# Optimization experiments

Hardware: AMD Instinct MI355X
Metric: run time of the kernel (lower is better)

## Reference

```python
import jax, jax.numpy as jnp
import numpy as np

NEG_INF = -1000000.0
B_, NG, HEADS, C, GH, GW, GD = 256, 64, 6, 192, 6, 6, 6
N = GH * GW * GD
POS_DIM = (C // 4) // 4  # DynamicPosBias(dim//4): pos_dim = (dim//4)//4 = 12


def setup_inputs() -> dict:
    key = jax.random.key(0)
    ks = jax.random.split(key, 12)
    rn = lambda k, shape, s=0.02: jax.random.normal(k, shape, jnp.float32) * s
    x = jax.random.normal(ks[0], (B_, N, C), jnp.float32)
    y = jax.random.normal(ks[1], (B_, N, C), jnp.float32)
    # 0 / -1e6 window mask, as produced by the padding logic upstream
    mask = jnp.where(jax.random.bernoulli(ks[2], 0.1, (NG, N, N)), NEG_INF, 0.0).astype(jnp.float32)
    return dict(
        x=x, y=y, mask=mask,
        Wqkv=rn(ks[3], (3 * C, C)), bqkv=jnp.zeros((3 * C,), jnp.float32),
        Wproj=rn(ks[4], (C, C)), bproj=jnp.zeros((C,), jnp.float32),
        pos_proj_w=rn(ks[5], (POS_DIM, 3)), pos_proj_b=jnp.zeros((POS_DIM,), jnp.float32),
        ln1_g=jnp.ones((POS_DIM,), jnp.float32), ln1_b=jnp.zeros((POS_DIM,), jnp.float32),
        pos1_w=rn(ks[6], (POS_DIM, POS_DIM)), pos1_b=jnp.zeros((POS_DIM,), jnp.float32),
        ln2_g=jnp.ones((POS_DIM,), jnp.float32), ln2_b=jnp.zeros((POS_DIM,), jnp.float32),
        pos2_w=rn(ks[7], (POS_DIM, POS_DIM)), pos2_b=jnp.zeros((POS_DIM,), jnp.float32),
        ln3_g=jnp.ones((POS_DIM,), jnp.float32), ln3_b=jnp.zeros((POS_DIM,), jnp.float32),
        pos3_w=rn(ks[8], (HEADS, POS_DIM)), pos3_b=jnp.zeros((HEADS,), jnp.float32),
        H=GH, W=GW, D=GD)


def _ln(t, g, b):
    m = t.mean(-1, keepdims=True)
    v = ((t - m) ** 2).mean(-1, keepdims=True)
    return (t - m) / jnp.sqrt(v + 1e-5) * g + b


def _rel_tables(H, W, D):
    # biases: all relative offsets in [1-H,H-1]x[1-W,W-1]x[1-D,D-1], shape (M, 3)
    ph = np.arange(1 - H, H); pw = np.arange(1 - W, W); pd = np.arange(1 - D, D)
    biases = np.stack(np.meshgrid(ph, pw, pd, indexing='ij')).reshape(3, -1).T.astype(np.float32)
    coords = np.stack(np.meshgrid(np.arange(H), np.arange(W), np.arange(D), indexing='ij')).reshape(3, -1)
    rel = (coords[:, :, None] - coords[:, None, :]).transpose(1, 2, 0)  # (N, N, 3)
    rel[..., 0] += H - 1; rel[..., 1] += W - 1; rel[..., 2] += D - 1
    rel[..., 0] *= (2 * W - 1) * (2 * D - 1); rel[..., 1] *= (2 * D - 1)
    idx = rel.sum(-1)  # (N, N) indices into the (M,) bias table
    return jnp.asarray(biases), jnp.asarray(idx)


def reference(x, y, mask, Wqkv, bqkv, Wproj, bproj, pos_proj_w, pos_proj_b,
              ln1_g, ln1_b, pos1_w, pos1_b, ln2_g, ln2_b, pos2_w, pos2_b,
              ln3_g, ln3_b, pos3_w, pos3_b, H, W, D):
    Bt, n, c = x.shape
    heads = pos3_w.shape[0]
    hd = c // heads
    scale = hd ** (-0.5)
    # NOTE: original code applies self.qkv to BOTH x and y (qkv_y layer unused)
    qkv = (x @ Wqkv.T + bqkv).reshape(Bt, n, 3, heads, hd).transpose(2, 0, 3, 1, 4)
    qkv_y = (y @ Wqkv.T + bqkv).reshape(Bt, n, 3, heads, hd).transpose(2, 0, 3, 1, 4)
    q = qkv[0] * scale
    k_y, v_y = qkv_y[1], qkv_y[2]
    attn = jnp.einsum('bhnd,bhmd->bhnm', q, k_y)
    # dynamic relative position bias: tiny MLP over offsets, then gather
    biases, idx = _rel_tables(H, W, D)
    pos = biases @ pos_proj_w.T + pos_proj_b
    pos = jnp.maximum(_ln(pos, ln1_g, ln1_b), 0) @ pos1_w.T + pos1_b
    pos = jnp.maximum(_ln(pos, ln2_g, ln2_b), 0) @ pos2_w.T + pos2_b
    pos = jnp.maximum(_ln(pos, ln3_g, ln3_b), 0) @ pos3_w.T + pos3_b  # (M, heads)
    rpb = pos[idx.reshape(-1)].reshape(n, n, heads).transpose(2, 0, 1)  # (heads, N, N)
    attn = attn + rpb[None]
    nG = mask.shape[0]
    attn = attn.reshape(Bt // nG, nG, heads, n, n) + mask[None, :, None]
    attn = jax.nn.softmax(attn, axis=-1).reshape(Bt, heads, n, n)
    out = jnp.einsum('bhnm,bhmd->bhnd', attn, v_y).transpose(0, 2, 1, 3).reshape(Bt, n, c)
    return out @ Wproj.T + bproj
```

## Files before the change

kernel.cpp:

```cpp
#include <hip/hip_runtime.h>
#include <stdint.h>

using short8   = __attribute__((ext_vector_type(8))) short;
using short4_  = __attribute__((ext_vector_type(4))) short;
using float4_  = __attribute__((ext_vector_type(4))) float;
using ushort4_ = __attribute__((ext_vector_type(4))) unsigned short;
typedef unsigned int  uint;
typedef unsigned short ushort;

__device__ __forceinline__ float bf2f(ushort b) {
  uint u = ((uint)b) << 16;
  return __builtin_bit_cast(float, u);
}
__device__ __forceinline__ ushort f2bf(float f) {
  uint u = __builtin_bit_cast(uint, f);
  u = u + 0x7fffu + ((u >> 16) & 1u);
  return (ushort)(u >> 16);
}
__device__ __forceinline__ float exp2_hw(float x) {
  float r;
  asm("v_exp_f32 %0, %1" : "=v"(r) : "v"(x));
  return r;
}
__device__ __forceinline__ void gld_lds16(const ushort* g, ushort* l) {
  __builtin_amdgcn_global_load_lds(
      (const __attribute__((address_space(1))) void*)g,
      (__attribute__((address_space(3))) void*)l, 16, 0, 0);
}
__device__ __forceinline__ int detect_f32(const uint* __restrict__ det) {
  int lane = threadIdx.x & 63;
  uint w = det[lane];
  ushort lo = (ushort)(w & 0xffffu);
  int e = (lo >> 7) & 0xff;
  int sane = (lo == 0 || (e >= 0x60 && e <= 0x9f)) ? 1 : 0;
  unsigned long long b = __ballot(sane);
  return (__popcll(b) >= 56) ? 0 : 1;
}

#define LOG2E 1.4426950408889634f

#define NN   216
#define NSQ  46656
#define PADV (-3.0e6f)

#if __has_builtin(__builtin_amdgcn_mfma_f32_16x16x16bf16_1k)
  #define HAVE_MFMA16 1
  #define MFMA16(a, b, c) __builtin_amdgcn_mfma_f32_16x16x16bf16_1k(a, b, c, 0, 0, 0)
#elif __has_builtin(__builtin_amdgcn_mfma_f32_16x16x16_bf16)
  #define HAVE_MFMA16 1
  #define MFMA16(a, b, c) __builtin_amdgcn_mfma_f32_16x16x16_bf16(a, b, c, 0, 0, 0)
#else
  #define HAVE_MFMA16 0
#endif

#define WA_WQKV   0
#define WA_BQKV   110592
#define WA_WPROJ  111168
#define WA_BPROJ  148032
#define WA_PPW    148224
#define WA_PPB    148260
#define WA_G1     148272
#define WA_B1     148284
#define WA_W1     148296
#define WA_WB1    148440
#define WA_G2     148452
#define WA_B2     148464
#define WA_W2     148476
#define WA_WB2    148620
#define WA_G3     148632
#define WA_B3     148644
#define WA_W3     148656
#define WA_WB3    148728
#define WA_TOTAL  148740

struct SrcPtrs { const void* p[18]; };

__global__ __launch_bounds__(256) void convpack_kernel(
    SrcPtrs sp, const uint* __restrict__ det,
    ushort* __restrict__ warena, ushort* __restrict__ wp) {
  int fl = detect_f32(det);
  int bid = blockIdx.x, tid = threadIdx.x;
  if (bid < 72) {
    int c = bid * 256 + tid;
    int blob = c / 2304, s = c - blob * 2304;
    int kk = s / 384, r = s - kk * 384;
    int nt = r >> 6, l = r & 63;
    int l16 = l & 15, qd = l >> 4;
    int col; const void* src;
    if (blob < 6) { int z = blob >> 1, half = blob & 1;
                    col = z * 192 + half * 96 + nt * 16 + l16; src = sp.p[0]; }
    else          { col = (blob - 6) * 96 + nt * 16 + l16;     src = sp.p[2]; }
    size_t off = (size_t)col * 192 + kk * 32 + qd * 8;
    short8 pk;
    if (fl) {
      float4_ lo = *(const float4_*)((const float*)src + off);
      float4_ hi = *(const float4_*)((const float*)src + off + 4);
#pragma unroll
      for (int j = 0; j < 4; ++j) {
        pk[j]     = (short)f2bf(lo[j]);
        pk[4 + j] = (short)f2bf(hi[j]);
      }
    } else {
      pk = *(const short8*)((const ushort*)src + off);
    }
    *(short8*)(wp + (size_t)c * 8) = pk;
  } else {
    constexpr int OFF[19] = {WA_WQKV, WA_BQKV, WA_WPROJ, WA_BPROJ, WA_PPW, WA_PPB,
                             WA_G1, WA_B1, WA_W1, WA_WB1, WA_G2, WA_B2, WA_W2,
                             WA_WB2, WA_G3, WA_B3, WA_W3, WA_WB3, WA_TOTAL};
    int u = (bid - 72) * 256 + tid;
    if (u >= 1284) return;
    int t, a;
    if (u < 576) { t = WA_BQKV + u; a = 1; }
    else {
      t = WA_BPROJ + (u - 576);
      a = 3;
#pragma unroll
      for (int i = 4; i < 18; ++i) a += (t >= OFF[i]) ? 1 : 0;
    }
    int local = t - OFF[a];
    const void* s = sp.p[a];
    warena[t] = fl ? f2bf(((const float*)s)[local]) : ((const ushort*)s)[local];
  }
}

__global__ __launch_bounds__(256) void packa_kernel(const void* __restrict__ src,
                                                    ushort* __restrict__ dst) {
  int fl = detect_f32((const uint*)src);
  int c = blockIdx.x * 256 + threadIdx.x;
  int tile = c / 3072, cc = c - tile * 3072;
  int kk = cc / 512, c2 = cc - kk * 512;
  int rowhi = c2 / 64, c3 = c2 - rowhi * 64;
  int q = c3 >> 4, l16 = c3 & 15;
  size_t M = (size_t)tile * 128 + rowhi * 16 + l16;
  size_t so = M * 192 + kk * 32 + q * 8;
  short8 pk;
  if (fl) {
    float4_ lo = *(const float4_*)((const float*)src + so);
    float4_ hi = *(const float4_*)((const float*)src + so + 4);
#pragma unroll
    for (int j = 0; j < 4; ++j) {
      pk[j]     = (short)f2bf(lo[j]);
      pk[4 + j] = (short)f2bf(hi[j]);
    }
  } else {
    pk = *(const short8*)((const ushort*)src + so);
  }
  *(short8*)(dst + (size_t)c * 8) = pk;
}

__device__ __forceinline__ void ln_relu(const float* p, const ushort* g,
                                        const ushort* b, float* r) {
  float m = 0.f;
#pragma unroll
  for (int t = 0; t < 12; ++t) m += p[t];
  m *= (1.f / 12.f);
  float v = 0.f;
#pragma unroll
  for (int t = 0; t < 12; ++t) { float d = p[t] - m; v += d * d; }
  v *= (1.f / 12.f);
  float inv = rsqrtf(v + 1e-5f);
#pragma unroll
  for (int t = 0; t < 12; ++t) {
    float z = (p[t] - m) * inv * bf2f(g[t]) + bf2f(b[t]);
    r[t] = fmaxf(z, 0.f);
  }
}

__global__ void pos_mlp_kernel(const ushort* __restrict__ wa, float* __restrict__ pos) {
  int m = blockIdx.x * blockDim.x + threadIdx.x;
  if (m >= 1331) return;
  const ushort* pw  = wa + WA_PPW;  const ushort* pb  = wa + WA_PPB;
  const ushort* g1  = wa + WA_G1;   const ushort* b1  = wa + WA_B1;
  const ushort* w1  = wa + WA_W1;   const ushort* wb1 = wa + WA_WB1;
  const ushort* g2  = wa + WA_G2;   const ushort* b2  = wa + WA_B2;
  const ushort* w2  = wa + WA_W2;   const ushort* wb2 = wa + WA_WB2;
  const ushort* g3  = wa + WA_G3;   const ushort* b3  = wa + WA_B3;
  const ushort* w3  = wa + WA_W3;   const ushort* wb3 = wa + WA_WB3;

  int ih = m / 121, rem = m - ih * 121;
  int iw = rem / 11, id = rem - iw * 11;
  float fh = (float)(ih - 5), fw = (float)(iw - 5), fd = (float)(id - 5);
  float p[12], r[12], q[12];
#pragma unroll
  for (int t = 0; t < 12; ++t)
    p[t] = fh * bf2f(pw[t * 3]) + fw * bf2f(pw[t * 3 + 1]) +
           fd * bf2f(pw[t * 3 + 2]) + bf2f(pb[t]);
  ln_relu(p, g1, b1, r);
#pragma unroll
  for (int t = 0; t < 12; ++t) {
    float s = bf2f(wb1[t]);
#pragma unroll
    for (int u = 0; u < 12; ++u) s += r[u] * bf2f(w1[t * 12 + u]);
    q[t] = s;
  }
  ln_relu(q, g2, b2, r);
#pragma unroll
  for (int t = 0; t < 12; ++t) {
    float s = bf2f(wb2[t]);
#pragma unroll
    for (int u = 0; u < 12; ++u) s += r[u] * bf2f(w2[t * 12 + u]);
    p[t] = s;
  }
  ln_relu(p, g3, b3, r);
#pragma unroll
  for (int h = 0; h < 6; ++h) {
    float s = bf2f(wb3[h]);
#pragma unroll
    for (int u = 0; u < 12; ++u) s += r[u] * bf2f(w3[h * 12 + u]);
    pos[m * 6 + h] = s;
  }
}

__global__ void rpbfrag_kernel(const float* __restrict__ pos, ushort* __restrict__ out) {
  int tgl = blockIdx.x * 256 + threadIdx.x;
  if (tgl >= 6 * 196 * 64) return;
  int lane = tgl & 63;
  int tj   = (tgl >> 6) % 196;
  int h    = (tgl >> 6) / 196;
  int tt = tj / 14, jt = tj - tt * 14;
  int l16 = lane & 15, quad = lane >> 4;
  int i = tt * 16 + l16;
  int jbase = jt * 16 + quad * 4;
  ushort4_ o;
  if (i < 216 && jbase < 216) {
    int h1 = i / 36, r1 = i - h1 * 36, w1 = r1 / 6, d1 = r1 - w1 * 6;
#pragma unroll
    for (int r = 0; r < 4; ++r) {
      int j = jbase + r;
      int h2 = j / 36, r2 = j - h2 * 36, w2 = r2 / 6, d2 = r2 - w2 * 6;
      int idx = ((h1 - h2 + 5) * 11 + (w1 - w2 + 5)) * 11 + (d1 - d2 + 5);
      o[r] = f2bf(pos[idx * 6 + h] * LOG2E);
    }
  } else {
#pragma unroll
    for (int r = 0; r < 4; ++r) o[r] = f2bf(PADV);
  }
  *(ushort4_*)(out + (size_t)tgl * 4) = o;
}

__global__ void maskfrag_kernel(const void* __restrict__ maskv,
                                const uint* __restrict__ det,
                                ushort* __restrict__ out) {
  bool mf32 = detect_f32(det) != 0;
  int tgl = blockIdx.x * 256 + threadIdx.x;
  if (tgl >= 64 * 196 * 64) return;
  int lane = tgl & 63;
  int tj   = (tgl >> 6) % 196;
  int g    = (tgl >> 6) / 196;
  int tt = tj / 14, jt = tj - tt * 14;
  int l16 = lane & 15, quad = lane >> 4;
  int i = tt * 16 + l16;
  int jbase = jt * 16 + quad * 4;
  ushort4_ o;
  if (i < 216 && jbase < 216) {
    int mi = i * 216 + jbase;
    if (mf32) {
      float4_ mv = *(const float4_*)((const float*)maskv + (size_t)g * NSQ + mi);
#pragma unroll
      for (int r = 0; r < 4; ++r) o[r] = f2bf(mv[r] * LOG2E);
    } else {
      ushort4_ raw = *(const ushort4_*)((const ushort*)maskv + (size_t)g * NSQ + mi);
#pragma unroll
      for (int r = 0; r < 4; ++r) o[r] = f2bf(bf2f(raw[r]) * LOG2E);
    }
  } else {
#pragma unroll
    for (int r = 0; r < 4; ++r) o[r] = f2bf(PADV);
  }
  *(ushort4_*)(out + (size_t)tgl * 4) = o;
}

template<int NT, int IS_PROJ>
__global__ __launch_bounds__(256, 2) void gemm_kernel(
    const void* __restrict__ Arow,
    const ushort* __restrict__ Apack,
    const ushort* __restrict__ wpacked,
    const ushort* __restrict__ bias,
    void* __restrict__ dq, void* __restrict__ dk, void* __restrict__ dv,
    const uint* __restrict__ det) {
  __shared__ __align__(16) ushort b_lds[NT * 3072];

  int fl = detect_f32(det);
  int tid = threadIdx.x;
  int tile = blockIdx.x;
  int m0 = tile * 128;
  int zz = blockIdx.y;
  int n0   = IS_PROJ ? zz * 96 : 0;
  int blob = IS_PROJ ? (6 + zz) : (zz * 2);
  float scale = (!IS_PROJ && zz == 0) ? (0.17677669529663687f * LOG2E) : 1.0f;
  void* dst = IS_PROJ ? dq : (zz == 0 ? dq : (zz == 1 ? dk : dv));
  bool a_packed = (!IS_PROJ) && (zz != 0);
  bool f32path = (!IS_PROJ) && (zz == 0) && (fl != 0);
  bool o_f32 = IS_PROJ && (fl != 0);

  int lane = tid & 63, w = tid >> 6;
  int l16 = lane & 15, quad = lane >> 4;

  {
    const ushort* wb = wpacked + (size_t)blob * 18432;
    int wuni = (tid >> 6) << 6;
#pragma unroll
    for (int it = 0; it < (NT * 3) / 2; ++it) {
      int base = wuni + it * 256;
      gld_lds16(wb + (size_t)(base + lane) * 8, b_lds + (size_t)base * 8);
    }
  }

  short8 af[6][2];
  if (a_packed) {
    const ushort* tb = Apack + (size_t)tile * 24576 + lane * 8;
#pragma unroll
    for (int kk = 0; kk < 6; ++kk)
#pragma unroll
      for (int mt = 0; mt < 2; ++mt)
        af[kk][mt] = *(const short8*)(tb + kk * 4096 + (w * 2 + mt) * 512);
  } else if (f32path) {
#pragma unroll
    for (int kk = 0; kk < 6; ++kk)
#pragma unroll
      for (int mt = 0; mt < 2; ++mt) {
        const float* Af = (const float*)Arow +
            (size_t)(m0 + w * 32 + mt * 16 + l16) * 192 + kk * 32 + quad * 8;
        float4_ lo = *(const float4_*)Af;
        float4_ hi = *(const float4_*)(Af + 4);
#pragma unroll
        for (int j = 0; j < 4; ++j) {
          af[kk][mt][j]     = (short)f2bf(lo[j]);
          af[kk][mt][4 + j] = (short)f2bf(hi[j]);
        }
      }
  } else {
#pragma unroll
    for (int kk = 0; kk < 6; ++kk)
#pragma unroll
      for (int mt = 0; mt < 2; ++mt)
        af[kk][mt] = *(const short8*)((const ushort*)Arow +
            (size_t)(m0 + w * 32 + mt * 16 + l16) * 192 + kk * 32 + quad * 8);
  }
  __syncthreads();

  float4_ acc[2][NT];
#pragma unroll
  for (int mt = 0; mt < 2; ++mt)
#pragma unroll
    for (int nt = 0; nt < NT; ++nt) acc[mt][nt] = (float4_){0.f, 0.f, 0.f, 0.f};

#pragma unroll
  for (int kk = 0; kk < 6; ++kk) {
    short8 bfr[NT];
#pragma unroll
    for (int nt = 0; nt < NT; ++nt) {
      int halfb = nt / 6, nl = nt % 6;
      bfr[nt] = *(const short8*)(b_lds + halfb * 18432 + ((kk * 6 + nl) * 64 + lane) * 8);
    }
#pragma unroll
    for (int mt = 0; mt < 2; ++mt)
#pragma unroll
      for (int nt = 0; nt < NT; ++nt)
        acc[mt][nt] = __builtin_amdgcn_mfma_f32_16x16x32_bf16(af[kk][mt], bfr[nt], acc[mt][nt], 0, 0, 0);
  }

#pragma unroll
  for (int mt = 0; mt < 2; ++mt) {
#pragma unroll
    for (int nt = 0; nt < NT; ++nt) {
      int lcol = n0 + nt * 16 + l16;
      float bv = bf2f(bias[(IS_PROJ ? 0 : zz * 192) + lcol]);
#pragma unroll
      for (int r = 0; r < 4; ++r) {
        int grow = m0 + w * 32 + mt * 16 + quad * 4 + r;
        float val = (acc[mt][nt][r] + bv) * scale;
        if (IS_PROJ) {
          if (o_f32) ((float*)dst)[(size_t)grow * 192 + lcol] = val;
          else       ((ushort*)dst)[(size_t)grow * 192 + lcol] = f2bf(val);
        } else {
          int bb = grow / 216;
          int nn2 = grow - bb * 216;
          int hh = lcol >> 5, dd = lcol & 31;
          ((ushort*)dst)[(((size_t)bb * 6 + hh) * 216 + nn2) * 32 + dd] = f2bf(val);
        }
      }
    }
  }
}

__global__ __launch_bounds__(448) void attn_kernel(
    const ushort* __restrict__ q, const ushort* __restrict__ k,
    const ushort* __restrict__ v, const ushort* __restrict__ rpbf,
    const ushort* __restrict__ maskf, ushort* __restrict__ opre) {
#if HAVE_MFMA16
  __shared__ __align__(16) ushort vfrag[28 * 64 * 4];
#else
  __shared__ __align__(16) ushort vfrag[14 * 64 * 8];
#endif

  int bid = blockIdx.x;
  int g   = bid / 24;
  int rr  = bid - g * 24;
  int bhi = rr / 6;
  int h   = rr - bhi * 6;
  int b   = bhi * 64 + g;

  int tid = threadIdx.x, lane = tid & 63, w = tid >> 6;
  int l16 = lane & 15, quad = lane >> 4;

  const ushort* qh = q + (size_t)(b * 6 + h) * 6912;
  const ushort* kh = k + (size_t)(b * 6 + h) * 6912;
  const ushort* vh = v + (size_t)(b * 6 + h) * 6912;

#if HAVE_MFMA16
  for (int pos = tid; pos < 1792; pos += 448) {
    int chunk = pos >> 6, l = pos & 63;
    int kt = chunk >> 1, dh = chunk & 1;
    int qd = l >> 4, lv = l & 15;
    ushort4_ tmp;
#pragma unroll
    for (int j = 0; j < 4; ++j)
      tmp[j] = vh[(kt * 16 + qd * 4 + j) * 32 + dh * 16 + lv];
    *(ushort4_*)(vfrag + pos * 4) = tmp;
  }
#else
  for (int pos = tid; pos < 896; pos += 448) {
    int chunk = pos >> 6, l = pos & 63;
    int kt2 = chunk >> 1, dh = chunk & 1;
    int qd = l >> 4, lv = l & 15;
    short8 tmp;
#pragma unroll
    for (int j = 0; j < 8; ++j)
      tmp[j] = (short)vh[(kt2 * 32 + qd * 8 + j) * 32 + dh * 16 + lv];
    *(short8*)(vfrag + pos * 8) = tmp;
  }
#endif
  __syncthreads();

  for (int t = w; t < 14; t += 7) {
    int r0 = t * 16;
    const ushort* rf = rpbf  + ((size_t)(h * 196 + t * 14) * 64 + lane) * 4;
    const ushort* mf = maskf + ((size_t)(g * 196 + t * 14) * 64 + lane) * 4;
    short8 aq = *(const short8*)(qh + (r0 + l16) * 32 + quad * 8);

    float4_ st[14];
#pragma unroll
    for (int jt = 0; jt < 14; ++jt) {
      ushort4_ rb = *(const ushort4_*)(rf + jt * 256);
      ushort4_ mb = *(const ushort4_*)(mf + jt * 256);
      float4_ cin;
#pragma unroll
      for (int r = 0; r < 4; ++r) cin[r] = bf2f(rb[r]) + bf2f(mb[r]);
      short8 bk = *(const short8*)(kh + (jt * 16 + l16) * 32 + quad * 8);
      st[jt] = __builtin_amdgcn_mfma_f32_16x16x32_bf16(bk, aq, cin, 0, 0, 0);
    }

    float mx = -1e30f;
#pragma unroll
    for (int jt = 0; jt < 14; ++jt)
      mx = fmaxf(fmaxf(st[jt][0], st[jt][1]),
                 fmaxf(fmaxf(st[jt][2], st[jt][3]), mx));
    mx = fmaxf(mx, __shfl_xor(mx, 16));
    mx = fmaxf(mx, __shfl_xor(mx, 32));
    float sum = 0.f;
#pragma unroll
    for (int jt = 0; jt < 14; ++jt)
#pragma unroll
      for (int r = 0; r < 4; ++r) {
        float pe = exp2_hw(st[jt][r] - mx);
        st[jt][r] = pe;
        sum += pe;
      }
    sum += __shfl_xor(sum, 16);
    sum += __shfl_xor(sum, 32);
    float inv = 1.0f / sum;

    float4_ o0 = (float4_){0.f, 0.f, 0.f, 0.f};
    float4_ o1 = (float4_){0.f, 0.f, 0.f, 0.f};

#if HAVE_MFMA16
#pragma unroll
    for (int kt = 0; kt < 14; ++kt) {
      short4_ pa;
#pragma unroll
      for (int r = 0; r < 4; ++r) pa[r] = (short)f2bf(st[kt][r]);
      short4_ vb0 = *(const short4_*)(vfrag + ((kt * 2 + 0) * 64 + lane) * 4);
      short4_ vb1 = *(const short4_*)(vfrag + ((kt * 2 + 1) * 64 + lane) * 4);
      o0 = MFMA16(pa, vb0, o0);
      o1 = MFMA16(pa, vb1, o1);
    }
#else
#pragma unroll
    for (int kt2 = 0; kt2 < 7; ++kt2) {
      uint pe0 = ((uint)f2bf(st[2*kt2][0])) | (((uint)f2bf(st[2*kt2][1])) << 16);
      uint pe1 = ((uint)f2bf(st[2*kt2][2])) | (((uint)f2bf(st[2*kt2][3])) << 16);
      uint po0 = ((uint)f2bf(st[2*kt2+1][0])) | (((uint)f2bf(st[2*kt2+1][1])) << 16);
      uint po1 = ((uint)f2bf(st[2*kt2+1][2])) | (((uint)f2bf(st[2*kt2+1][3])) << 16);
      int slo = (((2 * quad) & 3) << 4) | l16;
      int shi = (((2 * quad + 1) & 3) << 4) | l16;
      uint e_lo0 = __shfl((int)pe0, slo), e_lo1 = __shfl((int)pe1, slo);
      uint o_lo0 = __shfl((int)po0, slo), o_lo1 = __shfl((int)po1, slo);
      uint e_hi0 = __shfl((int)pe0, shi), e_hi1 = __shfl((int)pe1, shi);
      uint o_hi0 = __shfl((int)po0, shi), o_hi1 = __shfl((int)po1, shi);
      uint lo0 = (quad < 2) ? e_lo0 : o_lo0, lo1 = (quad < 2) ? e_lo1 : o_lo1;
      uint hi0 = (quad < 2) ? e_hi0 : o_hi0, hi1 = (quad < 2) ? e_hi1 : o_hi1;
      uint4 paw = {lo0, lo1, hi0, hi1};
      short8 pa = __builtin_bit_cast(short8, paw);
      short8 vb0 = *(const short8*)(vfrag + ((kt2 * 2 + 0) * 64 + lane) * 8);
      short8 vb1 = *(const short8*)(vfrag + ((kt2 * 2 + 1) * 64 + lane) * 8);
      o0 = __builtin_amdgcn_mfma_f32_16x16x32_bf16(pa, vb0, o0, 0, 0, 0);
      o1 = __builtin_amdgcn_mfma_f32_16x16x32_bf16(pa, vb1, o1, 0, 0, 0);
    }
#endif

#pragma unroll
    for (int r = 0; r < 4; ++r) {
      float ir = __shfl(inv, quad * 4 + r);
      int i = r0 + quad * 4 + r;
      if (i < 216) {
        size_t base = ((size_t)b * 216 + i) * 192 + h * 32;
        opre[base + l16]      = f2bf(o0[r] * ir);
        opre[base + 16 + l16] = f2bf(o1[r] * ir);
      }
    }
  }
}

extern "C" void kernel_launch(void* const* d_in, const int* in_sizes, int n_in,
                              void* d_out, int out_size, void* d_ws, size_t ws_size,
                              hipStream_t stream) {
  (void)in_sizes; (void)n_in; (void)out_size; (void)ws_size;

  char* p = (char*)d_ws;
  p += 256;
  ushort* warena  = (ushort*)p;        p += 298240;
  ushort* wpacked = (ushort*)p;        p += 294912;
  float*  pos     = (float*)p;         p += 32768;
  ushort* rpbf    = (ushort*)p;        p += 602112;
  ushort* maskf   = (ushort*)p;        p += 6422528;
  ushort* yf      = (ushort*)p;        p += 21234688;
  ushort* qb      = (ushort*)p;        p += 21234688;
  ushort* kb      = (ushort*)p;        p += 21234688;
  ushort* vb      = (ushort*)p;
  ushort* opre    = yf;

  const uint* xdet = (const uint*)d_in[0];

  SrcPtrs sp;
  for (int i = 0; i < 18; ++i) sp.p[i] = d_in[3 + i];

  convpack_kernel<<<78, 256, 0, stream>>>(sp, xdet, warena, wpacked);

  packa_kernel<<<5184, 256, 0, stream>>>(d_in[1], yf);

  pos_mlp_kernel<<<6, 256, 0, stream>>>(warena, pos);
  rpbfrag_kernel<<<294, 256, 0, stream>>>(pos, rpbf);
  maskfrag_kernel<<<3136, 256, 0, stream>>>(d_in[2], xdet, maskf);

  gemm_kernel<12, 0><<<dim3(432, 3), 256, 0, stream>>>(
      d_in[0], yf, wpacked, warena + WA_BQKV, qb, kb, vb, xdet);

  attn_kernel<<<1536, 448, 0, stream>>>(qb, kb, vb, rpbf, maskf, opre);

  gemm_kernel<6, 1><<<dim3(432, 2), 256, 0, stream>>>(
      opre, yf, wpacked, warena + WA_BPROJ,
      d_out, d_out, d_out, xdet);
}
```

Measured before the change: 285.4 us.

## Eliminate pre-pass kernels: read y and mask directly, fuse pos MLP into rpb

Removes the packa kernel so the QKV GEMM reads y directly through the same row path used for x. Removes the maskfrag kernel so the attention kernel loads the raw mask per tile and folds the LOG2E scale and padding into the bias input. The pos MLP is recomputed inside every rpbfrag block into shared memory, which saves a launch but repeats the MLP work in each of the 294 blocks. The aim is to cut launches and the intermediate global buffers, in exchange for less coalesced mask reads and extra per-block MLP compute.

Result: slower. 406.9 us (+42.6%).

```diff
diff --git a/kernel.cpp b/kernel.cpp
--- a/kernel.cpp
+++ b/kernel.cpp
@@ -124,31 +124,6 @@
   }
 }
 
-__global__ __launch_bounds__(256) void packa_kernel(const void* __restrict__ src,
-                                                    ushort* __restrict__ dst) {
-  int fl = detect_f32((const uint*)src);
-  int c = blockIdx.x * 256 + threadIdx.x;
-  int tile = c / 3072, cc = c - tile * 3072;
-  int kk = cc / 512, c2 = cc - kk * 512;
-  int rowhi = c2 / 64, c3 = c2 - rowhi * 64;
-  int q = c3 >> 4, l16 = c3 & 15;
-  size_t M = (size_t)tile * 128 + rowhi * 16 + l16;
-  size_t so = M * 192 + kk * 32 + q * 8;
-  short8 pk;
-  if (fl) {
-    float4_ lo = *(const float4_*)((const float*)src + so);
-    float4_ hi = *(const float4_*)((const float*)src + so + 4);
-#pragma unroll
-    for (int j = 0; j < 4; ++j) {
-      pk[j]     = (short)f2bf(lo[j]);
-      pk[4 + j] = (short)f2bf(hi[j]);
-    }
-  } else {
-    pk = *(const short8*)((const ushort*)src + so);
-  }
-  *(short8*)(dst + (size_t)c * 8) = pk;
-}
-
 __device__ __forceinline__ void ln_relu(const float* p, const ushort* g,
                                         const ushort* b, float* r) {
   float m = 0.f;
@@ -167,53 +142,56 @@
   }
 }
 
-__global__ void pos_mlp_kernel(const ushort* __restrict__ wa, float* __restrict__ pos) {
-  int m = blockIdx.x * blockDim.x + threadIdx.x;
-  if (m >= 1331) return;
-  const ushort* pw  = wa + WA_PPW;  const ushort* pb  = wa + WA_PPB;
-  const ushort* g1  = wa + WA_G1;   const ushort* b1  = wa + WA_B1;
-  const ushort* w1  = wa + WA_W1;   const ushort* wb1 = wa + WA_WB1;
-  const ushort* g2  = wa + WA_G2;   const ushort* b2  = wa + WA_B2;
-  const ushort* w2  = wa + WA_W2;   const ushort* wb2 = wa + WA_WB2;
-  const ushort* g3  = wa + WA_G3;   const ushort* b3  = wa + WA_B3;
-  const ushort* w3  = wa + WA_W3;   const ushort* wb3 = wa + WA_WB3;
-
-  int ih = m / 121, rem = m - ih * 121;
-  int iw = rem / 11, id = rem - iw * 11;
-  float fh = (float)(ih - 5), fw = (float)(iw - 5), fd = (float)(id - 5);
-  float p[12], r[12], q[12];
-#pragma unroll
-  for (int t = 0; t < 12; ++t)
-    p[t] = fh * bf2f(pw[t * 3]) + fw * bf2f(pw[t * 3 + 1]) +
-           fd * bf2f(pw[t * 3 + 2]) + bf2f(pb[t]);
-  ln_relu(p, g1, b1, r);
-#pragma unroll
-  for (int t = 0; t < 12; ++t) {
-    float s = bf2f(wb1[t]);
-#pragma unroll
-    for (int u = 0; u < 12; ++u) s += r[u] * bf2f(w1[t * 12 + u]);
-    q[t] = s;
-  }
-  ln_relu(q, g2, b2, r);
-#pragma unroll
-  for (int t = 0; t < 12; ++t) {
-    float s = bf2f(wb2[t]);
-#pragma unroll
-    for (int u = 0; u < 12; ++u) s += r[u] * bf2f(w2[t * 12 + u]);
-    p[t] = s;
-  }
-  ln_relu(p, g3, b3, r);
-#pragma unroll
-  for (int h = 0; h < 6; ++h) {
-    float s = bf2f(wb3[h]);
-#pragma unroll
-    for (int u = 0; u < 12; ++u) s += r[u] * bf2f(w3[h * 12 + u]);
-    pos[m * 6 + h] = s;
-  }
-}
-
-__global__ void rpbfrag_kernel(const float* __restrict__ pos, ushort* __restrict__ out) {
-  int tgl = blockIdx.x * 256 + threadIdx.x;
+__global__ __launch_bounds__(256) void rpbfrag_kernel(const ushort* __restrict__ wa,
+                                                      ushort* __restrict__ out) {
+  __shared__ float pos_l[1331 * 6];
+  int tid = threadIdx.x;
+  {
+    const ushort* pw  = wa + WA_PPW;  const ushort* pb  = wa + WA_PPB;
+    const ushort* g1  = wa + WA_G1;   const ushort* b1  = wa + WA_B1;
+    const ushort* w1  = wa + WA_W1;   const ushort* wb1 = wa + WA_WB1;
+    const ushort* g2  = wa + WA_G2;   const ushort* b2  = wa + WA_B2;
+    const ushort* w2  = wa + WA_W2;   const ushort* wb2 = wa + WA_WB2;
+    const ushort* g3  = wa + WA_G3;   const ushort* b3  = wa + WA_B3;
+    const ushort* w3  = wa + WA_W3;   const ushort* wb3 = wa + WA_WB3;
+    for (int m = tid; m < 1331; m += 256) {
+      int ih = m / 121, rem = m - ih * 121;
+      int iw = rem / 11, id = rem - iw * 11;
+      float fh = (float)(ih - 5), fw = (float)(iw - 5), fd = (float)(id - 5);
+      float p[12], r[12], q[12];
+#pragma unroll
+      for (int t = 0; t < 12; ++t)
+        p[t] = fh * bf2f(pw[t * 3]) + fw * bf2f(pw[t * 3 + 1]) +
+               fd * bf2f(pw[t * 3 + 2]) + bf2f(pb[t]);
+      ln_relu(p, g1, b1, r);
+#pragma unroll
+      for (int t = 0; t < 12; ++t) {
+        float s = bf2f(wb1[t]);
+#pragma unroll
+        for (int u = 0; u < 12; ++u) s += r[u] * bf2f(w1[t * 12 + u]);
+        q[t] = s;
+      }
+      ln_relu(q, g2, b2, r);
+#pragma unroll
+      for (int t = 0; t < 12; ++t) {
+        float s = bf2f(wb2[t]);
+#pragma unroll
+        for (int u = 0; u < 12; ++u) s += r[u] * bf2f(w2[t * 12 + u]);
+        p[t] = s;
+      }
+      ln_relu(p, g3, b3, r);
+#pragma unroll
+      for (int hh = 0; hh < 6; ++hh) {
+        float s = bf2f(wb3[hh]);
+#pragma unroll
+        for (int u = 0; u < 12; ++u) s += r[u] * bf2f(w3[hh * 12 + u]);
+        pos_l[m * 6 + hh] = s;
+      }
+    }
+  }
+  __syncthreads();
+
+  int tgl = blockIdx.x * 256 + tid;
   if (tgl >= 6 * 196 * 64) return;
   int lane = tgl & 63;
   int tj   = (tgl >> 6) % 196;
@@ -230,39 +208,7 @@
       int j = jbase + r;
       int h2 = j / 36, r2 = j - h2 * 36, w2 = r2 / 6, d2 = r2 - w2 * 6;
       int idx = ((h1 - h2 + 5) * 11 + (w1 - w2 + 5)) * 11 + (d1 - d2 + 5);
-      o[r] = f2bf(pos[idx * 6 + h] * LOG2E);
-    }
-  } else {
-#pragma unroll
-    for (int r = 0; r < 4; ++r) o[r] = f2bf(PADV);
-  }
-  *(ushort4_*)(out + (size_t)tgl * 4) = o;
-}
-
-__global__ void maskfrag_kernel(const void* __restrict__ maskv,
-                                const uint* __restrict__ det,
-                                ushort* __restrict__ out) {
-  bool mf32 = detect_f32(det) != 0;
-  int tgl = blockIdx.x * 256 + threadIdx.x;
-  if (tgl >= 64 * 196 * 64) return;
-  int lane = tgl & 63;
-  int tj   = (tgl >> 6) % 196;
-  int g    = (tgl >> 6) / 196;
-  int tt = tj / 14, jt = tj - tt * 14;
-  int l16 = lane & 15, quad = lane >> 4;
-  int i = tt * 16 + l16;
-  int jbase = jt * 16 + quad * 4;
-  ushort4_ o;
-  if (i < 216 && jbase < 216) {
-    int mi = i * 216 + jbase;
-    if (mf32) {
-      float4_ mv = *(const float4_*)((const float*)maskv + (size_t)g * NSQ + mi);
-#pragma unroll
-      for (int r = 0; r < 4; ++r) o[r] = f2bf(mv[r] * LOG2E);
-    } else {
-      ushort4_ raw = *(const ushort4_*)((const ushort*)maskv + (size_t)g * NSQ + mi);
-#pragma unroll
-      for (int r = 0; r < 4; ++r) o[r] = f2bf(bf2f(raw[r]) * LOG2E);
+      o[r] = f2bf(pos_l[idx * 6 + h] * LOG2E);
     }
   } else {
 #pragma unroll
@@ -273,8 +219,8 @@
 
 template<int NT, int IS_PROJ>
 __global__ __launch_bounds__(256, 2) void gemm_kernel(
-    const void* __restrict__ Arow,
-    const ushort* __restrict__ Apack,
+    const void* __restrict__ Ax,
+    const void* __restrict__ Ay,
     const ushort* __restrict__ wpacked,
     const ushort* __restrict__ bias,
     void* __restrict__ dq, void* __restrict__ dk, void* __restrict__ dv,
@@ -290,8 +236,8 @@
   int blob = IS_PROJ ? (6 + zz) : (zz * 2);
   float scale = (!IS_PROJ && zz == 0) ? (0.17677669529663687f * LOG2E) : 1.0f;
   void* dst = IS_PROJ ? dq : (zz == 0 ? dq : (zz == 1 ? dk : dv));
-  bool a_packed = (!IS_PROJ) && (zz != 0);
-  bool f32path = (!IS_PROJ) && (zz == 0) && (fl != 0);
+  const void* Arow = (!IS_PROJ && zz != 0) ? Ay : Ax;
+  bool f32path = (!IS_PROJ) && (fl != 0);
   bool o_f32 = IS_PROJ && (fl != 0);
 
   int lane = tid & 63, w = tid >> 6;
@@ -308,14 +254,7 @@
   }
 
   short8 af[6][2];
-  if (a_packed) {
-    const ushort* tb = Apack + (size_t)tile * 24576 + lane * 8;
-#pragma unroll
-    for (int kk = 0; kk < 6; ++kk)
-#pragma unroll
-      for (int mt = 0; mt < 2; ++mt)
-        af[kk][mt] = *(const short8*)(tb + kk * 4096 + (w * 2 + mt) * 512);
-  } else if (f32path) {
+  if (f32path) {
 #pragma unroll
     for (int kk = 0; kk < 6; ++kk)
 #pragma unroll
@@ -388,12 +327,15 @@
 __global__ __launch_bounds__(448) void attn_kernel(
     const ushort* __restrict__ q, const ushort* __restrict__ k,
     const ushort* __restrict__ v, const ushort* __restrict__ rpbf,
-    const ushort* __restrict__ maskf, ushort* __restrict__ opre) {
+    const void* __restrict__ maskv, const uint* __restrict__ det,
+    ushort* __restrict__ opre) {
 #if HAVE_MFMA16
   __shared__ __align__(16) ushort vfrag[28 * 64 * 4];
 #else
   __shared__ __align__(16) ushort vfrag[14 * 64 * 8];
 #endif
+
+  bool mf32 = detect_f32(det) != 0;
 
   int bid = blockIdx.x;
   int g   = bid / 24;
@@ -408,6 +350,8 @@
   const ushort* qh = q + (size_t)(b * 6 + h) * 6912;
   const ushort* kh = k + (size_t)(b * 6 + h) * 6912;
   const ushort* vh = v + (size_t)(b * 6 + h) * 6912;
+  const float*  mg32 = (const float*)maskv  + (size_t)g * NSQ;
+  const ushort* mg16 = (const ushort*)maskv + (size_t)g * NSQ;
 
 #if HAVE_MFMA16
   for (int pos = tid; pos < 1792; pos += 448) {
@@ -436,18 +380,31 @@
 
   for (int t = w; t < 14; t += 7) {
     int r0 = t * 16;
-    const ushort* rf = rpbf  + ((size_t)(h * 196 + t * 14) * 64 + lane) * 4;
-    const ushort* mf = maskf + ((size_t)(g * 196 + t * 14) * 64 + lane) * 4;
+    int i = r0 + l16;
+    bool iv = (i < 216);
+    int irow = iv ? i * 216 : 0;
+    const ushort* rf = rpbf + ((size_t)(h * 196 + t * 14) * 64 + lane) * 4;
     short8 aq = *(const short8*)(qh + (r0 + l16) * 32 + quad * 8);
 
     float4_ st[14];
 #pragma unroll
     for (int jt = 0; jt < 14; ++jt) {
       ushort4_ rb = *(const ushort4_*)(rf + jt * 256);
-      ushort4_ mb = *(const ushort4_*)(mf + jt * 256);
+      int j0 = jt * 16 + quad * 4;
+      bool vm = iv && (j0 < 216);
+      int mo = vm ? (irow + j0) : 0;
       float4_ cin;
-#pragma unroll
-      for (int r = 0; r < 4; ++r) cin[r] = bf2f(rb[r]) + bf2f(mb[r]);
+      if (mf32) {
+        float4_ mv = *(const float4_*)(mg32 + mo);
+#pragma unroll
+        for (int r = 0; r < 4; ++r)
+          cin[r] = vm ? fmaf(mv[r], LOG2E, bf2f(rb[r])) : (bf2f(rb[r]) + PADV);
+      } else {
+        ushort4_ mv = *(const ushort4_*)(mg16 + mo);
+#pragma unroll
+        for (int r = 0; r < 4; ++r)
+          cin[r] = vm ? fmaf(bf2f(mv[r]), LOG2E, bf2f(rb[r])) : (bf2f(rb[r]) + PADV);
+      }
       short8 bk = *(const short8*)(kh + (jt * 16 + l16) * 32 + quad * 8);
       st[jt] = __builtin_amdgcn_mfma_f32_16x16x32_bf16(bk, aq, cin, 0, 0, 0);
     }
@@ -513,9 +470,9 @@
 #pragma unroll
     for (int r = 0; r < 4; ++r) {
       float ir = __shfl(inv, quad * 4 + r);
-      int i = r0 + quad * 4 + r;
-      if (i < 216) {
-        size_t base = ((size_t)b * 216 + i) * 192 + h * 32;
+      int i2 = r0 + quad * 4 + r;
+      if (i2 < 216) {
+        size_t base = ((size_t)b * 216 + i2) * 192 + h * 32;
         opre[base + l16]      = f2bf(o0[r] * ir);
         opre[base + 16 + l16] = f2bf(o1[r] * ir);
       }
@@ -532,14 +489,13 @@
   p += 256;
   ushort* warena  = (ushort*)p;        p += 298240;
   ushort* wpacked = (ushort*)p;        p += 294912;
-  float*  pos     = (float*)p;         p += 32768;
+  p += 32768;
   ushort* rpbf    = (ushort*)p;        p += 602112;
-  ushort* maskf   = (ushort*)p;        p += 6422528;
-  ushort* yf      = (ushort*)p;        p += 21234688;
+  p += 6422528;
+  ushort* opre    = (ushort*)p;        p += 21234688;
   ushort* qb      = (ushort*)p;        p += 21234688;
   ushort* kb      = (ushort*)p;        p += 21234688;
   ushort* vb      = (ushort*)p;
-  ushort* opre    = yf;
 
   const uint* xdet = (const uint*)d_in[0];
 
@@ -548,18 +504,14 @@
 
   convpack_kernel<<<78, 256, 0, stream>>>(sp, xdet, warena, wpacked);
 
-  packa_kernel<<<5184, 256, 0, stream>>>(d_in[1], yf);
-
-  pos_mlp_kernel<<<6, 256, 0, stream>>>(warena, pos);
-  rpbfrag_kernel<<<294, 256, 0, stream>>>(pos, rpbf);
-  maskfrag_kernel<<<3136, 256, 0, stream>>>(d_in[2], xdet, maskf);
+  rpbfrag_kernel<<<294, 256, 0, stream>>>(warena, rpbf);
 
   gemm_kernel<12, 0><<<dim3(432, 3), 256, 0, stream>>>(
-      d_in[0], yf, wpacked, warena + WA_BQKV, qb, kb, vb, xdet);
-
-  attn_kernel<<<1536, 448, 0, stream>>>(qb, kb, vb, rpbf, maskf, opre);
+      d_in[0], d_in[1], wpacked, warena + WA_BQKV, qb, kb, vb, xdet);
+
+  attn_kernel<<<1536, 448, 0, stream>>>(qb, kb, vb, rpbf, d_in[2], xdet, opre);
 
   gemm_kernel<6, 1><<<dim3(432, 2), 256, 0, stream>>>(
-      opre, yf, wpacked, warena + WA_BPROJ,
+      opre, nullptr, wpacked, warena + WA_BPROJ,
       d_out, d_out, d_out, xdet);
 }
```
